# Kernel tuning notes

Hardware: AMD Instinct MI355X
Metric: run time of the kernel (lower is better)

The kernel has to match this reference:

```python
import jax, jax.numpy as jnp
import numpy as np

# Model config (matches init_kwargs)
V, SMAX, D, DH, H, M, L = 32000, 512, 512, 64, 8, 2048, 6
B, S, T = 4, 512, 512
PAD = 0

_SPEC = [
    ("tok_emb", (V, D), "n"), ("pos_emb", (SMAX, D), "n"),
    ("enc_ln1_w", (L, D), "1"), ("enc_ln1_b", (L, D), "0"),
    ("enc_wq", (L, H, D, DH), "n"), ("enc_wk", (L, H, D, DH), "n"), ("enc_wv", (L, H, D, DH), "n"),
    ("enc_wo", (L, H * DH, D), "n"), ("enc_bo", (L, D), "0"),
    ("enc_ln2_w", (L, D), "1"), ("enc_ln2_b", (L, D), "0"),
    ("enc_w1", (L, D, M), "n"), ("enc_b1", (L, M), "0"),
    ("enc_w2", (L, M, D), "n"), ("enc_b2", (L, D), "0"),
    ("enc_lnf_w", (D,), "1"), ("enc_lnf_b", (D,), "0"),
    ("dec_ln1_w", (L, D), "1"), ("dec_ln1_b", (L, D), "0"),
    ("dec_wq_s", (L, H, D, DH), "n"), ("dec_wk_s", (L, H, D, DH), "n"), ("dec_wv_s", (L, H, D, DH), "n"),
    ("dec_wo_s", (L, H * DH, D), "n"), ("dec_bo_s", (L, D), "0"),
    ("dec_ln2_w", (L, D), "1"), ("dec_ln2_b", (L, D), "0"),
    ("dec_wq_c", (L, H, D, DH), "n"), ("dec_wk_c", (L, H, D, DH), "n"), ("dec_wv_c", (L, H, D, DH), "n"),
    ("dec_wo_c", (L, H * DH, D), "n"), ("dec_bo_c", (L, D), "0"),
    ("dec_ln3_w", (L, D), "1"), ("dec_ln3_b", (L, D), "0"),
    ("dec_w1", (L, D, M), "n"), ("dec_b1", (L, M), "0"),
    ("dec_w2", (L, M, D), "n"), ("dec_b2", (L, D), "0"),
    ("dec_lnf_w", (D,), "1"), ("dec_lnf_b", (D,), "0"),
    ("head_w", (D, V), "n"), ("head_b", (V,), "0"),
]


def setup_inputs() -> dict:
    key = jax.random.key(0)
    k1, k2, key = jax.random.split(key, 3)
    inp = {
        "tokens_source": jax.random.randint(k1, (B, S), 0, V),
        "tokens_destination": jax.random.randint(k2, (B, T), 0, V),
    }
    for name, shape, kind in _SPEC:
        if kind == "n":
            key, k = jax.random.split(key)
            inp[name] = jax.random.normal(k, shape, jnp.float32) * 0.02
        elif kind == "1":
            inp[name] = jnp.ones(shape, jnp.float32)
        else:
            inp[name] = jnp.zeros(shape, jnp.float32)
    return inp


def _ln(x, w, b):
    mu = x.mean(-1, keepdims=True)
    var = ((x - mu) ** 2).mean(-1, keepdims=True)
    return (x - mu) * jax.lax.rsqrt(var + 1e-5) * w + b


def _mha(xq, xkv, wq, wk, wv, wo, bo, mask):
    # wq/wk/wv: [H, D, dh]; wo: [H*dh, D]; mask: bool [B or 1, Sq, Sk] (broadcast over heads)
    q = jnp.einsum("bsd,hde->bhse", xq, wq)
    k = jnp.einsum("btd,hde->bhte", xkv, wk)
    v = jnp.einsum("btd,hde->bhte", xkv, wv)
    scores = jnp.einsum("bhse,bhte->bhst", q, k) / (DH ** 0.5)
    scores = jnp.where(mask[:, None], scores, -jnp.inf)
    w = jax.nn.softmax(scores, axis=-1)
    o = jnp.einsum("bhst,bhte->bhse", w, v)
    b_, _, s_, _ = o.shape
    o = o.transpose(0, 2, 1, 3).reshape(b_, s_, H * DH)  # concat heads (head 0 first)
    return o @ wo + bo


def _forward(src, dst, p):
    s_, t_ = src.shape[1], dst.shape[1]
    key_mask = (src != PAD)[:, None, :]                      # [B,1,S]: mask over source keys
    causal = jnp.tril(jnp.ones((t_, t_), bool))[None]        # [1,T,T]
    x = p["tok_emb"][src] + p["pos_emb"][:s_]
    for i in range(L):
        h = _ln(x, p["enc_ln1_w"][i], p["enc_ln1_b"][i])
        x = x + _mha(h, h, p["enc_wq"][i], p["enc_wk"][i], p["enc_wv"][i], p["enc_wo"][i], p["enc_bo"][i], key_mask)
        h = _ln(x, p["enc_ln2_w"][i], p["enc_ln2_b"][i])
        x = x + jax.nn.gelu(h @ p["enc_w1"][i] + p["enc_b1"][i], approximate=False) @ p["enc_w2"][i] + p["enc_b2"][i]
    xe = _ln(x, p["enc_lnf_w"], p["enc_lnf_b"])
    y = p["tok_emb"][dst] + p["pos_emb"][:t_]
    for i in range(L):
        h = _ln(y, p["dec_ln1_w"][i], p["dec_ln1_b"][i])
        y = y + _mha(h, h, p["dec_wq_s"][i], p["dec_wk_s"][i], p["dec_wv_s"][i], p["dec_wo_s"][i], p["dec_bo_s"][i], causal)
        h = _ln(y, p["dec_ln2_w"][i], p["dec_ln2_b"][i])
        y = y + _mha(h, xe, p["dec_wq_c"][i], p["dec_wk_c"][i], p["dec_wv_c"][i], p["dec_wo_c"][i], p["dec_bo_c"][i], key_mask)
        h = _ln(y, p["dec_ln3_w"][i], p["dec_ln3_b"][i])
        y = y + jax.nn.gelu(h @ p["dec_w1"][i] + p["dec_b1"][i], approximate=False) @ p["dec_w2"][i] + p["dec_b2"][i]
    yd = _ln(y, p["dec_lnf_w"], p["dec_lnf_b"])
    return yd @ p["head_w"] + p["head_b"]  # logits [B, T, V]


def reference(tokens_source, tokens_destination, tok_emb, pos_emb, enc_ln1_w, enc_ln1_b, enc_wq, enc_wk, enc_wv, enc_wo, enc_bo, enc_ln2_w, enc_ln2_b, enc_w1, enc_b1, enc_w2, enc_b2, enc_lnf_w, enc_lnf_b, dec_ln1_w, dec_ln1_b, dec_wq_s, dec_wk_s, dec_wv_s, dec_wo_s, dec_bo_s, dec_ln2_w, dec_ln2_b, dec_wq_c, dec_wk_c, dec_wv_c, dec_wo_c, dec_bo_c, dec_ln3_w, dec_ln3_b, dec_w1, dec_b1, dec_w2, dec_b2, dec_lnf_w, dec_lnf_b, head_w, head_b):
    p = {k: v for k, v in locals().items() if k not in ("tokens_source", "tokens_destination")}
    return _forward(tokens_source, tokens_destination, p)
```

## Files before the change

### kernel.cpp

```cpp
#include <hip/hip_runtime.h>
#include <math.h>


typedef __bf16 bf16;
typedef bf16  bf16x8 __attribute__((ext_vector_type(8)));
typedef float f32x4  __attribute__((ext_vector_type(4)));

#define DEV __device__ __forceinline__

DEV f32x4 mfma16(bf16x8 a, bf16x8 b, f32x4 c) {
  return __builtin_amdgcn_mfma_f32_16x16x32_bf16(a, b, c, 0, 0, 0);
}

DEV void async_copy16(const bf16* g, bf16* l) {
  __builtin_amdgcn_global_load_lds(
      (__attribute__((address_space(1))) void*)(g),
      (__attribute__((address_space(3))) void*)(l), 16, 0, 0);
}

struct TJob { const float* in; bf16* out; long long oHi, oLo, oOfs; int R, C, zdiv, tile0; };
struct TJobs { TJob j[17]; };

__global__ __launch_bounds__(256) void tcast_all(TJobs JJ, int njobs)
{
  __shared__ float tile[32][33];
  const int t = blockIdx.x;
  int ji = 0;
#pragma unroll
  for (int k = 1; k < 17; ++k) if (k < njobs && JJ.j[k].tile0 <= t) ji = k;
  const TJob J = JJ.j[ji];
  const int rel  = t - J.tile0;
  const int ntx  = J.C >> 5, nty = J.R >> 5;
  const int perz = ntx * nty;
  const int z    = rel / perz;
  const int r2   = rel - z * perz;
  const int bx   = r2 % ntx, by = r2 / ntx;

  const long long zi = (long long)z * J.R * J.C;
  const long long zo = (long long)(z / J.zdiv) * J.oHi + (long long)(z % J.zdiv) * J.oLo + J.oOfs;
  const int c0 = bx * 32, r0 = by * 32;
  const int tx = threadIdx.x & 31, ty = (threadIdx.x >> 5);
#pragma unroll
  for (int i = 0; i < 32; i += 8)
    tile[ty + i][tx] = J.in[zi + (long long)(r0 + ty + i) * J.C + c0 + tx];
  __syncthreads();
#pragma unroll
  for (int i = 0; i < 32; i += 8)
    J.out[zo + (long long)(c0 + ty + i) * J.R + r0 + tx] = (bf16)tile[tx][ty + i];
}

__global__ __launch_bounds__(64) void embedln_kernel(
    const int* __restrict__ tok, const float* __restrict__ temb,
    const float* __restrict__ pemb, float* __restrict__ x,
    const float* __restrict__ w, const float* __restrict__ b,
    bf16* __restrict__ out)
{
  const int row  = blockIdx.x;
  const int sPos = row & 511;
  const int t    = tok[row];
  const int lane = threadIdx.x;
  const int c0   = lane * 8;
  f32x4 a0 = *(const f32x4*)&temb[(long long)t * 512 + c0];
  f32x4 a1 = *(const f32x4*)&temb[(long long)t * 512 + c0 + 4];
  f32x4 p0 = *(const f32x4*)&pemb[(long long)sPos * 512 + c0];
  f32x4 p1 = *(const f32x4*)&pemb[(long long)sPos * 512 + c0 + 4];
  a0 += p0; a1 += p1;
  *(f32x4*)&x[(long long)row * 512 + c0]     = a0;
  *(f32x4*)&x[(long long)row * 512 + c0 + 4] = a1;
  float s = 0.f, q = 0.f;
#pragma unroll
  for (int k = 0; k < 4; ++k) { s += a0[k] + a1[k]; q += a0[k]*a0[k] + a1[k]*a1[k]; }
#pragma unroll
  for (int m = 1; m < 64; m <<= 1) { s += __shfl_xor(s, m); q += __shfl_xor(q, m); }
  const float mean = s * (1.f / 512.f);
  const float var  = q * (1.f / 512.f) - mean * mean;
  const float rs   = rsqrtf(var + 1e-5f);
  f32x4 w0 = *(const f32x4*)&w[c0], w1 = *(const f32x4*)&w[c0 + 4];
  f32x4 b0 = *(const f32x4*)&b[c0], b1 = *(const f32x4*)&b[c0 + 4];
  bf16x8 o;
#pragma unroll
  for (int k = 0; k < 4; ++k) {
    o[k]     = (bf16)((a0[k] - mean) * rs * w0[k] + b0[k]);
    o[k + 4] = (bf16)((a1[k] - mean) * rs * w1[k] + b1[k]);
  }
  *(bf16x8*)&out[(long long)row * 512 + c0] = o;
}

__global__ __launch_bounds__(256) void addln_kernel(
    const bf16* __restrict__ g, const float* __restrict__ bias,
    float* __restrict__ x, const float* __restrict__ w,
    const float* __restrict__ bb, bf16* __restrict__ out)
{
  const int row  = blockIdx.x * 4 + (threadIdx.x >> 6);
  const int lane = threadIdx.x & 63;
  const int c0   = lane * 8;
  float* xr = x + (long long)row * 512;
  f32x4 a0 = *(const f32x4*)&xr[c0];
  f32x4 a1 = *(const f32x4*)&xr[c0 + 4];
  bf16x8 gv = *(const bf16x8*)&g[(long long)row * 512 + c0];
  f32x4 bi0 = *(const f32x4*)&bias[c0], bi1 = *(const f32x4*)&bias[c0 + 4];
  float v[8];
#pragma unroll
  for (int k = 0; k < 4; ++k) {
    v[k]     = a0[k] + (float)gv[k]     + bi0[k];
    v[k + 4] = a1[k] + (float)gv[k + 4] + bi1[k];
  }
  *(f32x4*)&xr[c0]     = f32x4{v[0], v[1], v[2], v[3]};
  *(f32x4*)&xr[c0 + 4] = f32x4{v[4], v[5], v[6], v[7]};
  float s = 0.f, q = 0.f;
#pragma unroll
  for (int k = 0; k < 8; ++k) { s += v[k]; q += v[k] * v[k]; }
#pragma unroll
  for (int m = 1; m < 64; m <<= 1) { s += __shfl_xor(s, m); q += __shfl_xor(q, m); }
  const float mean = s * (1.f / 512.f);
  const float var  = q * (1.f / 512.f) - mean * mean;
  const float rs   = rsqrtf(var + 1e-5f);
  f32x4 w0 = *(const f32x4*)&w[c0], w1 = *(const f32x4*)&w[c0 + 4];
  f32x4 b0 = *(const f32x4*)&bb[c0], b1 = *(const f32x4*)&bb[c0 + 4];
  bf16x8 o;
#pragma unroll
  for (int k = 0; k < 4; ++k) {
    o[k]     = (bf16)((v[k] - mean) * rs * w0[k] + b0[k]);
    o[k + 4] = (bf16)((v[k + 4] - mean) * rs * w1[k] + b1[k]);
  }
  *(bf16x8*)&out[(long long)row * 512 + c0] = o;
}

template <int MODE>
__global__ __launch_bounds__(64) void attn_kernel(
    const bf16* __restrict__ Q, const bf16* __restrict__ K,
    const bf16* __restrict__ Vt, bf16* __restrict__ O,
    const int* __restrict__ srctok)
{
  __shared__ bf16 Pw[16 * 68];
  const int bh = blockIdx.y;
  const int b  = bh >> 3;
  const int q0 = blockIdx.x * 16;
  const int ln = threadIdx.x;
  const int lr = ln & 15, g = ln >> 4;
  const bf16* Qg = Q + ((long long)bh * 512 + q0) * 64;
  const bf16* Kg = K + (long long)bh * 512 * 64;
  const bf16* Vg = Vt + (long long)bh * 64 * 512;
  const int* tkb = srctok + b * 512;

  const bf16x8 aq0 = *(const bf16x8*)&Qg[lr * 64 + g * 8];
  const bf16x8 aq1 = *(const bf16x8*)&Qg[lr * 64 + 32 + g * 8];

  float m[4] = {-1e30f, -1e30f, -1e30f, -1e30f};
  float l[4] = {0.f, 0.f, 0.f, 0.f};
  f32x4 o[4] = {};

  const int ktEnd = (MODE == 1) ? (q0 + 16) : 512;
  for (int kt = 0; kt < ktEnd; kt += 64) {
    bf16x8 bk[4][2], bv[4][2];
#pragma unroll
    for (int j = 0; j < 4; ++j) {
      bk[j][0] = *(const bf16x8*)&Kg[(long long)(kt + j * 16 + lr) * 64 + g * 8];
      bk[j][1] = *(const bf16x8*)&Kg[(long long)(kt + j * 16 + lr) * 64 + 32 + g * 8];
    }
#pragma unroll
    for (int n = 0; n < 4; ++n) {
      bv[n][0] = *(const bf16x8*)&Vg[(long long)(n * 16 + lr) * 512 + kt + g * 8];
      bv[n][1] = *(const bf16x8*)&Vg[(long long)(n * 16 + lr) * 512 + kt + 32 + g * 8];
    }
    f32x4 sf[4] = {};
#pragma unroll
    for (int j = 0; j < 4; ++j) {
      sf[j] = mfma16(aq0, bk[j][0], sf[j]);
      sf[j] = mfma16(aq1, bk[j][1], sf[j]);
    }
    float rm[4] = {-1e30f, -1e30f, -1e30f, -1e30f};
#pragma unroll
    for (int j = 0; j < 4; ++j) {
      if (MODE == 0) {
        const bool ok = (tkb[kt + j * 16 + lr] != 0);
#pragma unroll
        for (int r = 0; r < 4; ++r) if (!ok) sf[j][r] = -1e30f;
      } else {
        const int key = kt + j * 16 + lr;
#pragma unroll
        for (int r = 0; r < 4; ++r)
          if (key > q0 + g * 4 + r) sf[j][r] = -1e30f;
      }
#pragma unroll
      for (int r = 0; r < 4; ++r) rm[r] = fmaxf(rm[r], sf[j][r]);
    }
#pragma unroll
    for (int mk = 1; mk < 16; mk <<= 1)
#pragma unroll
      for (int r = 0; r < 4; ++r) rm[r] = fmaxf(rm[r], __shfl_xor(rm[r], mk));
    float al[4], ps[4] = {0.f, 0.f, 0.f, 0.f};
#pragma unroll
    for (int r = 0; r < 4; ++r) {
      const float mx = fmaxf(m[r], rm[r]);
      al[r] = __expf(m[r] - mx);
      m[r] = mx;
    }
#pragma unroll
    for (int j = 0; j < 4; ++j) {
#pragma unroll
      for (int r = 0; r < 4; ++r) {
        const float p = (sf[j][r] <= -1e29f) ? 0.f : __expf(sf[j][r] - m[r]);
        ps[r] += p;
        Pw[(g * 4 + r) * 68 + j * 16 + lr] = (bf16)p;
      }
    }
#pragma unroll
    for (int mk = 1; mk < 16; mk <<= 1)
#pragma unroll
      for (int r = 0; r < 4; ++r) ps[r] += __shfl_xor(ps[r], mk);
#pragma unroll
    for (int r = 0; r < 4; ++r) l[r] = l[r] * al[r] + ps[r];
#pragma unroll
    for (int n = 0; n < 4; ++n)
#pragma unroll
      for (int r = 0; r < 4; ++r) o[n][r] *= al[r];
#pragma unroll
    for (int ks = 0; ks < 2; ++ks) {
      const bf16x8 ap = *(const bf16x8*)&Pw[lr * 68 + ks * 32 + g * 8];
#pragma unroll
      for (int n = 0; n < 4; ++n)
        o[n] = mfma16(ap, bv[n][ks], o[n]);
    }
  }

#pragma unroll
  for (int r = 0; r < 4; ++r) {
    const float inv = 1.f / l[r];
    const long long gr = (long long)b * 512 + q0 + g * 4 + r;
#pragma unroll
    for (int n = 0; n < 4; ++n)
      O[gr * 512 + (bh & 7) * 64 + n * 16 + lr] = (bf16)(o[n][r] * inv);
  }
}

template <int BM, int BN, int EPI, bool SWZ = false>
__global__ __launch_bounds__(256) void gemm_kernel(
    const bf16* __restrict__ A, const bf16* __restrict__ Bw,
    void* __restrict__ Cc, const float* __restrict__ bias,
    const int K, const int lda, const int ldb, const int ldc,
    const long long sAz, const long long sBz,
    const long long sClo, const long long sChi, const int HB,
    const float scale)
{
  constexpr int BK = 64;
  __shared__ bf16 As[2][BM * BK];
  __shared__ bf16 Bs[2][BN * BK];
  constexpr int AISS = (BM * BK * 2) / 4096;
  constexpr int BISS = (BN * BK * 2) / 4096;

  const int z = blockIdx.z;
  const bf16* Az = A + (long long)z * sAz;
  const bf16* Bz = Bw + (long long)z * sBz;
  const long long cofs = (long long)(z % HB) * sClo + (long long)(z / HB) * sChi;

  const int tid  = threadIdx.x;
  const int wave = tid >> 6;
  const int lane = tid & 63;
  const int lr   = lane & 15;
  const int kg   = lane >> 4;

  int bx = blockIdx.x, by = blockIdx.y;
  if constexpr (SWZ) {
    const int nx = gridDim.x;
    const int nwg = nx * gridDim.y;
    const int id = by * nx + bx;
    const int chunk = nwg >> 3;
    const int swz = (id & 7) * chunk + (id >> 3);
    bx = swz % nx; by = swz / nx;
  }
  const int m0 = bx * BM;
  const int n0 = by * BN;

  constexpr int FM = BM / 32;
  constexpr int FN = BN / 32;
  const int wm = (wave >> 1) * (BM / 2);
  const int wn = (wave & 1) * (BN / 2);

  f32x4 acc[FM][FN] = {};

  auto stage = [&](int buf, int kt) {
#pragma unroll
    for (int i = 0; i < AISS; ++i) {
      const int o = i * 4096 + tid * 16;
      const int r = o >> 7;
      const int c = (o & 127) >> 1;
      async_copy16(Az + (long long)(m0 + r) * lda + kt + c, (bf16*)((char*)&As[buf][0] + o));
    }
#pragma unroll
    for (int i = 0; i < BISS; ++i) {
      const int o = i * 4096 + tid * 16;
      const int r = o >> 7;
      const int c = (o & 127) >> 1;
      async_copy16(Bz + (long long)(n0 + r) * ldb + kt + c, (bf16*)((char*)&Bs[buf][0] + o));
    }
  };

  const int NT = K / BK;
  stage(0, 0);
  asm volatile("s_waitcnt vmcnt(0)" ::: "memory");
  __builtin_amdgcn_s_barrier();
  __builtin_amdgcn_sched_barrier(0);

  int cur = 0;
  for (int t = 0; t < NT; ++t) {
    if (t + 1 < NT) stage(cur ^ 1, (t + 1) * BK);
#pragma unroll
    for (int ks = 0; ks < 2; ++ks) {
      bf16x8 af[FM], bq[FN];
#pragma unroll
      for (int i = 0; i < FM; ++i)
        af[i] = *(const bf16x8*)&As[cur][(wm + i * 16 + lr) * BK + ks * 32 + kg * 8];
#pragma unroll
      for (int j = 0; j < FN; ++j)
        bq[j] = *(const bf16x8*)&Bs[cur][(wn + j * 16 + lr) * BK + ks * 32 + kg * 8];
#pragma unroll
      for (int i = 0; i < FM; ++i)
#pragma unroll
        for (int j = 0; j < FN; ++j)
          acc[i][j] = mfma16(af[i], bq[j], acc[i][j]);
    }
    if (t + 1 < NT) {
      asm volatile("s_waitcnt vmcnt(0) lgkmcnt(0)" ::: "memory");
      __builtin_amdgcn_s_barrier();
      __builtin_amdgcn_sched_barrier(0);
      cur ^= 1;
    }
  }

#pragma unroll
  for (int i = 0; i < FM; ++i) {
#pragma unroll
    for (int j = 0; j < FN; ++j) {
      const int gc = n0 + wn + j * 16 + lr;
#pragma unroll
      for (int r = 0; r < 4; ++r) {
        const int gr = m0 + wm + i * 16 + kg * 4 + r;
        const float v = acc[i][j][r];
        if constexpr (EPI == 0) {
          ((bf16*)Cc + cofs)[(long long)gr * ldc + gc] = (bf16)v;
        } else if constexpr (EPI == 3) {
          float t = v + bias[gc];
          t = 0.5f * t * (1.f + erff(t * 0.70710678118654752f));
          ((bf16*)Cc)[(long long)gr * ldc + gc] = (bf16)t;
        } else if constexpr (EPI == 4) {
          __builtin_nontemporal_store(v + bias[gc], &((float*)Cc)[(long long)gr * ldc + gc]);
        } else if constexpr (EPI == 7) {
          const int sel = gc >> 9;
          const int hh = (gc >> 6) & 7, ee = gc & 63;
          const int bb = gr >> 9, ss = gr & 511;
          bf16* base = (bf16*)Cc + (long long)sel * (2048 * 512);
          const float vv = (sel == 0) ? v * 0.125f : v;
          if (sel < 2) base[(((long long)(bb * 8 + hh) << 9) + ss) * 64 + ee] = (bf16)vv;
          else         base[(((long long)(bb * 8 + hh) << 6) + ee) * 512 + ss] = (bf16)vv;
        } else if constexpr (EPI == 8) {
          const int sel = gc >> 9;
          const int hh = (gc >> 6) & 7, ee = gc & 63;
          const int bb = gr >> 9, ss = gr & 511;
          bf16* base = (bf16*)Cc + (long long)z * sChi + (long long)sel * (2048 * 512);
          if (sel == 0) base[(((long long)(bb * 8 + hh) << 9) + ss) * 64 + ee] = (bf16)v;
          else          base[(((long long)(bb * 8 + hh) << 6) + ee) * 512 + ss] = (bf16)v;
        }
      }
    }
  }
}

extern "C" void kernel_launch(void* const* d_in, const int* in_sizes, int n_in,
                              void* d_out, int out_size, void* d_ws, size_t ws_size,
                              hipStream_t stream)
{
  const int*   tok_src   = (const int*)d_in[0];
  const int*   tok_dst   = (const int*)d_in[1];
  const float* tok_emb   = (const float*)d_in[2];
  const float* pos_emb   = (const float*)d_in[3];
  const float* enc_ln1_w = (const float*)d_in[4];
  const float* enc_ln1_b = (const float*)d_in[5];
  const float* enc_wq    = (const float*)d_in[6];
  const float* enc_wk    = (const float*)d_in[7];
  const float* enc_wv    = (const float*)d_in[8];
  const float* enc_wo    = (const float*)d_in[9];
  const float* enc_bo    = (const float*)d_in[10];
  const float* enc_ln2_w = (const float*)d_in[11];
  const float* enc_ln2_b = (const float*)d_in[12];
  const float* enc_w1    = (const float*)d_in[13];
  const float* enc_b1    = (const float*)d_in[14];
  const float* enc_w2    = (const float*)d_in[15];
  const float* enc_b2    = (const float*)d_in[16];
  const float* enc_lnf_w = (const float*)d_in[17];
  const float* enc_lnf_b = (const float*)d_in[18];
  const float* dec_ln1_w = (const float*)d_in[19];
  const float* dec_ln1_b = (const float*)d_in[20];
  const float* dec_wq_s  = (const float*)d_in[21];
  const float* dec_wk_s  = (const float*)d_in[22];
  const float* dec_wv_s  = (const float*)d_in[23];
  const float* dec_wo_s  = (const float*)d_in[24];
  const float* dec_bo_s  = (const float*)d_in[25];
  const float* dec_ln2_w = (const float*)d_in[26];
  const float* dec_ln2_b = (const float*)d_in[27];
  const float* dec_wq_c  = (const float*)d_in[28];
  const float* dec_wk_c  = (const float*)d_in[29];
  const float* dec_wv_c  = (const float*)d_in[30];
  const float* dec_wo_c  = (const float*)d_in[31];
  const float* dec_bo_c  = (const float*)d_in[32];
  const float* dec_ln3_w = (const float*)d_in[33];
  const float* dec_ln3_b = (const float*)d_in[34];
  const float* dec_w1    = (const float*)d_in[35];
  const float* dec_b1    = (const float*)d_in[36];
  const float* dec_w2    = (const float*)d_in[37];
  const float* dec_b2    = (const float*)d_in[38];
  const float* dec_lnf_w = (const float*)d_in[39];
  const float* dec_lnf_b = (const float*)d_in[40];
  const float* head_w    = (const float*)d_in[41];
  const float* head_b    = (const float*)d_in[42];
  float* outp = (float*)d_out;

  char* wp = (char*)d_ws;
  auto alloc = [&](size_t nbytes) -> char* {
    char* p = wp; wp += (nbytes + 255) & ~(size_t)255; return p;
  };
  const long long LQKV = 1536LL * 512;
  const long long LKV  = 1024LL * 512;
  const long long LSQ  = 512LL * 512;
  const long long LFF  = 2048LL * 512;
  const long long KVST = 2LL * 2048 * 512;

  bf16* tQKV_e = (bf16*)alloc((size_t)6 * LQKV * 2);
  bf16* tQKV_s = (bf16*)alloc((size_t)6 * LQKV * 2);
  bf16* tQ_c   = (bf16*)alloc((size_t)6 * LSQ * 2);
  bf16* tKV_c  = (bf16*)alloc((size_t)6 * LKV * 2);
  bf16* tWo_e  = (bf16*)alloc((size_t)6 * LSQ * 2);
  bf16* tWo_s  = (bf16*)alloc((size_t)6 * LSQ * 2);
  bf16* tWo_c  = (bf16*)alloc((size_t)6 * LSQ * 2);
  bf16* tW1_e  = (bf16*)alloc((size_t)6 * LFF * 2);
  bf16* tW2_e  = (bf16*)alloc((size_t)6 * LFF * 2);
  bf16* tW1_d  = (bf16*)alloc((size_t)6 * LFF * 2);
  bf16* tW2_d  = (bf16*)alloc((size_t)6 * LFF * 2);
  bf16* tHead  = (bf16*)alloc((size_t)32000 * 512 * 2);

  float* x   = (float*)alloc((size_t)2048 * 512 * 4);
  float* y   = (float*)alloc((size_t)2048 * 512 * 4);
  bf16*  h   = (bf16*)alloc((size_t)2048 * 512 * 2);
  bf16*  qkv = (bf16*)alloc((size_t)3 * 2048 * 512 * 2);
  bf16*  xe  = (bf16*)alloc((size_t)2048 * 512 * 2);
  bf16*  kvc = (bf16*)alloc((size_t)6 * KVST * 2);
  bf16*  ob  = (bf16*)alloc((size_t)2048 * 512 * 2);
  bf16*  t0  = (bf16*)alloc((size_t)2048 * 512 * 2);
  bf16*  h1  = (bf16*)alloc((size_t)2048 * 2048 * 2);
  bf16*  yd  = (bf16*)alloc((size_t)2048 * 512 * 2);

  bf16* ql = qkv;
  bf16* kl = qkv + 2048 * 512;
  bf16* vt = qkv + 2 * 2048 * 512;

  TJobs JJ; int nt = 0, nj = 0;
  auto addjob = [&](const float* in, bf16* out, int R, int C,
                    long long oHi, long long oLo, int zdiv, long long oOfs, int nz) {
    JJ.j[nj] = TJob{in, out, oHi, oLo, oOfs, R, C, zdiv, nt};
    nt += (C / 32) * (R / 32) * nz; ++nj;
  };
  addjob(enc_wq,   tQKV_e, 512, 64,   LQKV, 32768, 8, 0,      48);
  addjob(enc_wk,   tQKV_e, 512, 64,   LQKV, 32768, 8, 262144, 48);
  addjob(enc_wv,   tQKV_e, 512, 64,   LQKV, 32768, 8, 524288, 48);
  addjob(dec_wq_s, tQKV_s, 512, 64,   LQKV, 32768, 8, 0,      48);
  addjob(dec_wk_s, tQKV_s, 512, 64,   LQKV, 32768, 8, 262144, 48);
  addjob(dec_wv_s, tQKV_s, 512, 64,   LQKV, 32768, 8, 524288, 48);
  addjob(dec_wq_c, tQ_c,   512, 64,   LSQ,  32768, 8, 0,      48);
  addjob(dec_wk_c, tKV_c,  512, 64,   LKV,  32768, 8, 0,      48);
  addjob(dec_wv_c, tKV_c,  512, 64,   LKV,  32768, 8, 262144, 48);
  addjob(enc_wo,   tWo_e,  512, 512,  LSQ,  0, 1, 0, 6);
  addjob(dec_wo_s, tWo_s,  512, 512,  LSQ,  0, 1, 0, 6);
  addjob(dec_wo_c, tWo_c,  512, 512,  LSQ,  0, 1, 0, 6);
  addjob(enc_w1,   tW1_e,  512, 2048, LFF,  0, 1, 0, 6);
  addjob(enc_w2,   tW2_e,  2048, 512, LFF,  0, 1, 0, 6);
  addjob(dec_w1,   tW1_d,  512, 2048, LFF,  0, 1, 0, 6);
  addjob(dec_w2,   tW2_d,  2048, 512, LFF,  0, 1, 0, 6);
  addjob(head_w,   tHead,  512, 32000, 0,   0, 1, 0, 1);
  tcast_all<<<nt, 256, 0, stream>>>(JJ, nj);

  embedln_kernel<<<2048, 64, 0, stream>>>(tok_src, tok_emb, pos_emb, x, enc_ln1_w, enc_ln1_b, h);
  for (int l = 0; l < 6; ++l) {
    gemm_kernel<64, 128, 7><<<dim3(32, 12, 1), 256, 0, stream>>>(
        h, tQKV_e + (size_t)l * LQKV, qkv, nullptr, 512, 512, 512, 0, 0, 0, 0, 0, 1, 1.f);
    attn_kernel<0><<<dim3(32, 32), 64, 0, stream>>>(ql, kl, vt, ob, tok_src);
    gemm_kernel<64, 64, 0><<<dim3(32, 8, 1), 256, 0, stream>>>(
        ob, tWo_e + (size_t)l * LSQ, t0, nullptr, 512, 512, 512, 512, 0, 0, 0, 0, 1, 1.f);
    addln_kernel<<<512, 256, 0, stream>>>(t0, enc_bo + l * 512, x,
        enc_ln2_w + l * 512, enc_ln2_b + l * 512, h);
    gemm_kernel<64, 128, 3><<<dim3(32, 16, 1), 256, 0, stream>>>(
        h, tW1_e + (size_t)l * LFF, h1, enc_b1 + l * 2048, 512, 512, 512, 2048, 0, 0, 0, 0, 1, 1.f);
    gemm_kernel<64, 64, 0><<<dim3(32, 8, 1), 256, 0, stream>>>(
        h1, tW2_e + (size_t)l * LFF, t0, nullptr, 2048, 2048, 2048, 512, 0, 0, 0, 0, 1, 1.f);
    const float* nw = (l < 5) ? enc_ln1_w + (l + 1) * 512 : enc_lnf_w;
    const float* nb = (l < 5) ? enc_ln1_b + (l + 1) * 512 : enc_lnf_b;
    addln_kernel<<<512, 256, 0, stream>>>(t0, enc_b2 + l * 512, x, nw, nb, (l < 5) ? h : xe);
  }

  gemm_kernel<128, 128, 8><<<dim3(16, 8, 6), 256, 0, stream>>>(
      xe, tKV_c, kvc, nullptr, 512, 512, 512, 0, 0, LKV, 0, KVST, 1, 1.f);

  embedln_kernel<<<2048, 64, 0, stream>>>(tok_dst, tok_emb, pos_emb, y, dec_ln1_w, dec_ln1_b, h);
  for (int l = 0; l < 6; ++l) {
    gemm_kernel<64, 128, 7><<<dim3(32, 12, 1), 256, 0, stream>>>(
        h, tQKV_s + (size_t)l * LQKV, qkv, nullptr, 512, 512, 512, 0, 0, 0, 0, 0, 1, 1.f);
    attn_kernel<1><<<dim3(32, 32), 64, 0, stream>>>(ql, kl, vt, ob, nullptr);
    gemm_kernel<64, 64, 0><<<dim3(32, 8, 1), 256, 0, stream>>>(
        ob, tWo_s + (size_t)l * LSQ, t0, nullptr, 512, 512, 512, 512, 0, 0, 0, 0, 1, 1.f);
    addln_kernel<<<512, 256, 0, stream>>>(t0, dec_bo_s + l * 512, y,
        dec_ln2_w + l * 512, dec_ln2_b + l * 512, h);
    gemm_kernel<64, 64, 7><<<dim3(32, 8, 1), 256, 0, stream>>>(
        h, tQ_c + (size_t)l * LSQ, qkv, nullptr, 512, 512, 512, 0, 0, 0, 0, 0, 1, 1.f);
    attn_kernel<0><<<dim3(32, 32), 64, 0, stream>>>(
        ql, kvc + (size_t)l * KVST, kvc + (size_t)l * KVST + 2048 * 512, ob, tok_src);
    gemm_kernel<64, 64, 0><<<dim3(32, 8, 1), 256, 0, stream>>>(
        ob, tWo_c + (size_t)l * LSQ, t0, nullptr, 512, 512, 512, 512, 0, 0, 0, 0, 1, 1.f);
    addln_kernel<<<512, 256, 0, stream>>>(t0, dec_bo_c + l * 512, y,
        dec_ln3_w + l * 512, dec_ln3_b + l * 512, h);
    gemm_kernel<64, 128, 3><<<dim3(32, 16, 1), 256, 0, stream>>>(
        h, tW1_d + (size_t)l * LFF, h1, dec_b1 + l * 2048, 512, 512, 512, 2048, 0, 0, 0, 0, 1, 1.f);
    gemm_kernel<64, 64, 0><<<dim3(32, 8, 1), 256, 0, stream>>>(
        h1, tW2_d + (size_t)l * LFF, t0, nullptr, 2048, 2048, 2048, 512, 0, 0, 0, 0, 1, 1.f);
    const float* nw = (l < 5) ? dec_ln1_w + (l + 1) * 512 : dec_lnf_w;
    const float* nb = (l < 5) ? dec_ln1_b + (l + 1) * 512 : dec_lnf_b;
    addln_kernel<<<512, 256, 0, stream>>>(t0, dec_b2 + l * 512, y, nw, nb, (l < 5) ? h : yd);
  }
  gemm_kernel<128, 128, 4, true><<<dim3(16, 250, 1), 256, 0, stream>>>(
      yd, tHead, outp, head_b, 512, 512, 512, 32000, 0, 0, 0, 0, 1, 1.f);
}
```

Before: 2.144 ms.

## Split-K output GEMMs into fp32 partials, shrink tiles, widen attention blocks

The Wo and W2 projection GEMMs now use split-K (2 or 4 slices), writing fp32 partial sums that the add+LayerNorm kernel adds together. This gives more blocks on the small-N GEMMs and drops the bf16 rounding of their outputs. The other GEMMs move to 32-row tiles for more blocks, attention processes 128 keys per iteration instead of 64, and the encoder and decoder embedding+LN are merged into one launch, with the decoder result staged in yd and copied to h later. The cost is extra partial-buffer traffic and higher register pressure in attention.

```diff
diff --git a/kernel.cpp b/kernel.cpp
--- a/kernel.cpp
+++ b/kernel.cpp
@@ -49,13 +49,22 @@
     J.out[zo + (long long)(c0 + ty + i) * J.R + r0 + tx] = (bf16)tile[tx][ty + i];
 }
 
-__global__ __launch_bounds__(64) void embedln_kernel(
-    const int* __restrict__ tok, const float* __restrict__ temb,
-    const float* __restrict__ pemb, float* __restrict__ x,
-    const float* __restrict__ w, const float* __restrict__ b,
-    bf16* __restrict__ out)
+__global__ __launch_bounds__(64) void embedln2_kernel(
+    const int* __restrict__ tokA, const int* __restrict__ tokB,
+    const float* __restrict__ temb, const float* __restrict__ pemb,
+    float* __restrict__ xA, float* __restrict__ xB,
+    const float* __restrict__ wA, const float* __restrict__ bA,
+    const float* __restrict__ wB, const float* __restrict__ bB,
+    bf16* __restrict__ outA, bf16* __restrict__ outB)
 {
-  const int row  = blockIdx.x;
+  const bool sB = blockIdx.x >= 2048;
+  const int row = sB ? blockIdx.x - 2048 : blockIdx.x;
+  const int* tok = sB ? tokB : tokA;
+  float* x = sB ? xB : xA;
+  const float* w = sB ? wB : wA;
+  const float* b = sB ? bB : bA;
+  bf16* out = sB ? outB : outA;
+
   const int sPos = row & 511;
   const int t    = tok[row];
   const int lane = threadIdx.x;
@@ -86,8 +95,9 @@
   *(bf16x8*)&out[(long long)row * 512 + c0] = o;
 }
 
+template <int P>
 __global__ __launch_bounds__(256) void addln_kernel(
-    const bf16* __restrict__ g, const float* __restrict__ bias,
+    const float* __restrict__ part, const float* __restrict__ bias,
     float* __restrict__ x, const float* __restrict__ w,
     const float* __restrict__ bb, bf16* __restrict__ out)
 {
@@ -97,19 +107,19 @@
   float* xr = x + (long long)row * 512;
   f32x4 a0 = *(const f32x4*)&xr[c0];
   f32x4 a1 = *(const f32x4*)&xr[c0 + 4];
-  bf16x8 gv = *(const bf16x8*)&g[(long long)row * 512 + c0];
+#pragma unroll
+  for (int p = 0; p < P; ++p) {
+    const float* pr = part + (long long)p * (2048 * 512) + (long long)row * 512;
+    a0 += *(const f32x4*)&pr[c0];
+    a1 += *(const f32x4*)&pr[c0 + 4];
+  }
   f32x4 bi0 = *(const f32x4*)&bias[c0], bi1 = *(const f32x4*)&bias[c0 + 4];
-  float v[8];
-#pragma unroll
-  for (int k = 0; k < 4; ++k) {
-    v[k]     = a0[k] + (float)gv[k]     + bi0[k];
-    v[k + 4] = a1[k] + (float)gv[k + 4] + bi1[k];
-  }
-  *(f32x4*)&xr[c0]     = f32x4{v[0], v[1], v[2], v[3]};
-  *(f32x4*)&xr[c0 + 4] = f32x4{v[4], v[5], v[6], v[7]};
+  a0 += bi0; a1 += bi1;
+  *(f32x4*)&xr[c0]     = a0;
+  *(f32x4*)&xr[c0 + 4] = a1;
   float s = 0.f, q = 0.f;
 #pragma unroll
-  for (int k = 0; k < 8; ++k) { s += v[k]; q += v[k] * v[k]; }
+  for (int k = 0; k < 4; ++k) { s += a0[k] + a1[k]; q += a0[k]*a0[k] + a1[k]*a1[k]; }
 #pragma unroll
   for (int m = 1; m < 64; m <<= 1) { s += __shfl_xor(s, m); q += __shfl_xor(q, m); }
   const float mean = s * (1.f / 512.f);
@@ -120,8 +130,8 @@
   bf16x8 o;
 #pragma unroll
   for (int k = 0; k < 4; ++k) {
-    o[k]     = (bf16)((v[k] - mean) * rs * w0[k] + b0[k]);
-    o[k + 4] = (bf16)((v[k + 4] - mean) * rs * w1[k] + b1[k]);
+    o[k]     = (bf16)((a0[k] - mean) * rs * w0[k] + b0[k]);
+    o[k + 4] = (bf16)((a1[k] - mean) * rs * w1[k] + b1[k]);
   }
   *(bf16x8*)&out[(long long)row * 512 + c0] = o;
 }
@@ -132,7 +142,7 @@
     const bf16* __restrict__ Vt, bf16* __restrict__ O,
     const int* __restrict__ srctok)
 {
-  __shared__ bf16 Pw[16 * 68];
+  __shared__ bf16 Pw[16 * 136];
   const int bh = blockIdx.y;
   const int b  = bh >> 3;
   const int q0 = blockIdx.x * 16;
@@ -151,27 +161,28 @@
   f32x4 o[4] = {};
 
   const int ktEnd = (MODE == 1) ? (q0 + 16) : 512;
-  for (int kt = 0; kt < ktEnd; kt += 64) {
-    bf16x8 bk[4][2], bv[4][2];
-#pragma unroll
-    for (int j = 0; j < 4; ++j) {
+  for (int kt = 0; kt < ktEnd; kt += 128) {
+    bf16x8 bk[8][2], bv[4][4];
+#pragma unroll
+    for (int j = 0; j < 8; ++j) {
       bk[j][0] = *(const bf16x8*)&Kg[(long long)(kt + j * 16 + lr) * 64 + g * 8];
       bk[j][1] = *(const bf16x8*)&Kg[(long long)(kt + j * 16 + lr) * 64 + 32 + g * 8];
     }
 #pragma unroll
-    for (int n = 0; n < 4; ++n) {
-      bv[n][0] = *(const bf16x8*)&Vg[(long long)(n * 16 + lr) * 512 + kt + g * 8];
-      bv[n][1] = *(const bf16x8*)&Vg[(long long)(n * 16 + lr) * 512 + kt + 32 + g * 8];
-    }
-    f32x4 sf[4] = {};
-#pragma unroll
-    for (int j = 0; j < 4; ++j) {
+    for (int n = 0; n < 4; ++n)
+#pragma unroll
+      for (int ks = 0; ks < 4; ++ks)
+        bv[n][ks] = *(const bf16x8*)&Vg[(long long)(n * 16 + lr) * 512 + kt + ks * 32 + g * 8];
+
+    f32x4 sf[8] = {};
+#pragma unroll
+    for (int j = 0; j < 8; ++j) {
       sf[j] = mfma16(aq0, bk[j][0], sf[j]);
       sf[j] = mfma16(aq1, bk[j][1], sf[j]);
     }
     float rm[4] = {-1e30f, -1e30f, -1e30f, -1e30f};
 #pragma unroll
-    for (int j = 0; j < 4; ++j) {
+    for (int j = 0; j < 8; ++j) {
       if (MODE == 0) {
         const bool ok = (tkb[kt + j * 16 + lr] != 0);
 #pragma unroll
@@ -197,12 +208,12 @@
       m[r] = mx;
     }
 #pragma unroll
-    for (int j = 0; j < 4; ++j) {
+    for (int j = 0; j < 8; ++j) {
 #pragma unroll
       for (int r = 0; r < 4; ++r) {
         const float p = (sf[j][r] <= -1e29f) ? 0.f : __expf(sf[j][r] - m[r]);
         ps[r] += p;
-        Pw[(g * 4 + r) * 68 + j * 16 + lr] = (bf16)p;
+        Pw[(g * 4 + r) * 136 + j * 16 + lr] = (bf16)p;
       }
     }
 #pragma unroll
@@ -216,8 +227,8 @@
 #pragma unroll
       for (int r = 0; r < 4; ++r) o[n][r] *= al[r];
 #pragma unroll
-    for (int ks = 0; ks < 2; ++ks) {
-      const bf16x8 ap = *(const bf16x8*)&Pw[lr * 68 + ks * 32 + g * 8];
+    for (int ks = 0; ks < 4; ++ks) {
+      const bf16x8 ap = *(const bf16x8*)&Pw[lr * 136 + ks * 32 + g * 8];
 #pragma unroll
       for (int n = 0; n < 4; ++n)
         o[n] = mfma16(ap, bv[n][ks], o[n]);
@@ -337,9 +348,7 @@
       for (int r = 0; r < 4; ++r) {
         const int gr = m0 + wm + i * 16 + kg * 4 + r;
         const float v = acc[i][j][r];
-        if constexpr (EPI == 0) {
-          ((bf16*)Cc + cofs)[(long long)gr * ldc + gc] = (bf16)v;
-        } else if constexpr (EPI == 3) {
+        if constexpr (EPI == 3) {
           float t = v + bias[gc];
           t = 0.5f * t * (1.f + erff(t * 0.70710678118654752f));
           ((bf16*)Cc)[(long long)gr * ldc + gc] = (bf16)t;
@@ -360,6 +369,8 @@
           bf16* base = (bf16*)Cc + (long long)z * sChi + (long long)sel * (2048 * 512);
           if (sel == 0) base[(((long long)(bb * 8 + hh) << 9) + ss) * 64 + ee] = (bf16)v;
           else          base[(((long long)(bb * 8 + hh) << 6) + ee) * 512 + ss] = (bf16)v;
+        } else if constexpr (EPI == 9) {
+          ((float*)Cc)[cofs + (long long)gr * ldc + gc] = v;
         }
       }
     }
@@ -424,6 +435,7 @@
   const long long LSQ  = 512LL * 512;
   const long long LFF  = 2048LL * 512;
   const long long KVST = 2LL * 2048 * 512;
+  const long long PSTR = 2048LL * 512;
 
   bf16* tQKV_e = (bf16*)alloc((size_t)6 * LQKV * 2);
   bf16* tQKV_s = (bf16*)alloc((size_t)6 * LQKV * 2);
@@ -438,16 +450,16 @@
   bf16* tW2_d  = (bf16*)alloc((size_t)6 * LFF * 2);
   bf16* tHead  = (bf16*)alloc((size_t)32000 * 512 * 2);
 
-  float* x   = (float*)alloc((size_t)2048 * 512 * 4);
-  float* y   = (float*)alloc((size_t)2048 * 512 * 4);
-  bf16*  h   = (bf16*)alloc((size_t)2048 * 512 * 2);
-  bf16*  qkv = (bf16*)alloc((size_t)3 * 2048 * 512 * 2);
-  bf16*  xe  = (bf16*)alloc((size_t)2048 * 512 * 2);
-  bf16*  kvc = (bf16*)alloc((size_t)6 * KVST * 2);
-  bf16*  ob  = (bf16*)alloc((size_t)2048 * 512 * 2);
-  bf16*  t0  = (bf16*)alloc((size_t)2048 * 512 * 2);
-  bf16*  h1  = (bf16*)alloc((size_t)2048 * 2048 * 2);
-  bf16*  yd  = (bf16*)alloc((size_t)2048 * 512 * 2);
+  float* x    = (float*)alloc((size_t)2048 * 512 * 4);
+  float* y    = (float*)alloc((size_t)2048 * 512 * 4);
+  bf16*  h    = (bf16*)alloc((size_t)2048 * 512 * 2);
+  bf16*  qkv  = (bf16*)alloc((size_t)3 * 2048 * 512 * 2);
+  bf16*  xe   = (bf16*)alloc((size_t)2048 * 512 * 2);
+  bf16*  kvc  = (bf16*)alloc((size_t)6 * KVST * 2);
+  bf16*  ob   = (bf16*)alloc((size_t)2048 * 512 * 2);
+  float* part = (float*)alloc((size_t)4 * PSTR * 4);
+  bf16*  h1   = (bf16*)alloc((size_t)2048 * 2048 * 2);
+  bf16*  yd   = (bf16*)alloc((size_t)2048 * 512 * 2);
 
   bf16* ql = qkv;
   bf16* kl = qkv + 2048 * 512;
@@ -478,51 +490,55 @@
   addjob(head_w,   tHead,  512, 32000, 0,   0, 1, 0, 1);
   tcast_all<<<nt, 256, 0, stream>>>(JJ, nj);
 
-  embedln_kernel<<<2048, 64, 0, stream>>>(tok_src, tok_emb, pos_emb, x, enc_ln1_w, enc_ln1_b, h);
+  embedln2_kernel<<<4096, 64, 0, stream>>>(tok_src, tok_dst, tok_emb, pos_emb,
+      x, y, enc_ln1_w, enc_ln1_b, dec_ln1_w, dec_ln1_b, h, yd);
+
   for (int l = 0; l < 6; ++l) {
-    gemm_kernel<64, 128, 7><<<dim3(32, 12, 1), 256, 0, stream>>>(
+    gemm_kernel<32, 128, 7><<<dim3(64, 12, 1), 256, 0, stream>>>(
         h, tQKV_e + (size_t)l * LQKV, qkv, nullptr, 512, 512, 512, 0, 0, 0, 0, 0, 1, 1.f);
     attn_kernel<0><<<dim3(32, 32), 64, 0, stream>>>(ql, kl, vt, ob, tok_src);
-    gemm_kernel<64, 64, 0><<<dim3(32, 8, 1), 256, 0, stream>>>(
-        ob, tWo_e + (size_t)l * LSQ, t0, nullptr, 512, 512, 512, 512, 0, 0, 0, 0, 1, 1.f);
-    addln_kernel<<<512, 256, 0, stream>>>(t0, enc_bo + l * 512, x,
+    gemm_kernel<32, 64, 9><<<dim3(64, 8, 2), 256, 0, stream>>>(
+        ob, tWo_e + (size_t)l * LSQ, part, nullptr, 256, 512, 512, 512, 256, 256, 0, PSTR, 1, 1.f);
+    addln_kernel<2><<<512, 256, 0, stream>>>(part, enc_bo + l * 512, x,
         enc_ln2_w + l * 512, enc_ln2_b + l * 512, h);
-    gemm_kernel<64, 128, 3><<<dim3(32, 16, 1), 256, 0, stream>>>(
+    gemm_kernel<32, 128, 3><<<dim3(64, 16, 1), 256, 0, stream>>>(
         h, tW1_e + (size_t)l * LFF, h1, enc_b1 + l * 2048, 512, 512, 512, 2048, 0, 0, 0, 0, 1, 1.f);
-    gemm_kernel<64, 64, 0><<<dim3(32, 8, 1), 256, 0, stream>>>(
-        h1, tW2_e + (size_t)l * LFF, t0, nullptr, 2048, 2048, 2048, 512, 0, 0, 0, 0, 1, 1.f);
+    gemm_kernel<32, 64, 9><<<dim3(64, 8, 4), 256, 0, stream>>>(
+        h1, tW2_e + (size_t)l * LFF, part, nullptr, 512, 2048, 2048, 512, 512, 512, 0, PSTR, 1, 1.f);
     const float* nw = (l < 5) ? enc_ln1_w + (l + 1) * 512 : enc_lnf_w;
     const float* nb = (l < 5) ? enc_ln1_b + (l + 1) * 512 : enc_lnf_b;
-    addln_kernel<<<512, 256, 0, stream>>>(t0, enc_b2 + l * 512, x, nw, nb, (l < 5) ? h : xe);
+    addln_kernel<4><<<512, 256, 0, stream>>>(part, enc_b2 + l * 512, x, nw, nb, (l < 5) ? h : xe);
   }
 
   gemm_kernel<128, 128, 8><<<dim3(16, 8, 6), 256, 0, stream>>>(
       xe, tKV_c, kvc, nullptr, 512, 512, 512, 0, 0, LKV, 0, KVST, 1, 1.f);
 
-  embedln_kernel<<<2048, 64, 0, stream>>>(tok_dst, tok_emb, pos_emb, y, dec_ln1_w, dec_ln1_b, h);
+  {
+    hipMemcpyAsync(h, yd, (size_t)2048 * 512 * 2, hipMemcpyDeviceToDevice, stream);
+  }
   for (int l = 0; l < 6; ++l) {
-    gemm_kernel<64, 128, 7><<<dim3(32, 12, 1), 256, 0, stream>>>(
+    gemm_kernel<32, 128, 7><<<dim3(64, 12, 1), 256, 0, stream>>>(
         h, tQKV_s + (size_t)l * LQKV, qkv, nullptr, 512, 512, 512, 0, 0, 0, 0, 0, 1, 1.f);
     attn_kernel<1><<<dim3(32, 32), 64, 0, stream>>>(ql, kl, vt, ob, nullptr);
-    gemm_kernel<64, 64, 0><<<dim3(32, 8, 1), 256, 0, stream>>>(
-        ob, tWo_s + (size_t)l * LSQ, t0, nullptr, 512, 512, 512, 512, 0, 0, 0, 0, 1, 1.f);
-    addln_kernel<<<512, 256, 0, stream>>>(t0, dec_bo_s + l * 512, y,
+    gemm_kernel<32, 64, 9><<<dim3(64, 8, 2), 256, 0, stream>>>(
+        ob, tWo_s + (size_t)l * LSQ, part, nullptr, 256, 512, 512, 512, 256, 256, 0, PSTR, 1, 1.f);
+    addln_kernel<2><<<512, 256, 0, stream>>>(part, dec_bo_s + l * 512, y,
         dec_ln2_w + l * 512, dec_ln2_b + l * 512, h);
-    gemm_kernel<64, 64, 7><<<dim3(32, 8, 1), 256, 0, stream>>>(
+    gemm_kernel<32, 64, 7><<<dim3(64, 8, 1), 256, 0, stream>>>(
         h, tQ_c + (size_t)l * LSQ, qkv, nullptr, 512, 512, 512, 0, 0, 0, 0, 0, 1, 1.f);
     attn_kernel<0><<<dim3(32, 32), 64, 0, stream>>>(
         ql, kvc + (size_t)l * KVST, kvc + (size_t)l * KVST + 2048 * 512, ob, tok_src);
-    gemm_kernel<64, 64, 0><<<dim3(32, 8, 1), 256, 0, stream>>>(
-        ob, tWo_c + (size_t)l * LSQ, t0, nullptr, 512, 512, 512, 512, 0, 0, 0, 0, 1, 1.f);
-    addln_kernel<<<512, 256, 0, stream>>>(t0, dec_bo_c + l * 512, y,
+    gemm_kernel<32, 64, 9><<<dim3(64, 8, 2), 256, 0, stream>>>(
+        ob, tWo_c + (size_t)l * LSQ, part, nullptr, 256, 512, 512, 512, 256, 256, 0, PSTR, 1, 1.f);
+    addln_kernel<2><<<512, 256, 0, stream>>>(part, dec_bo_c + l * 512, y,
         dec_ln3_w + l * 512, dec_ln3_b + l * 512, h);
-    gemm_kernel<64, 128, 3><<<dim3(32, 16, 1), 256, 0, stream>>>(
+    gemm_kernel<32, 128, 3><<<dim3(64, 16, 1), 256, 0, stream>>>(
         h, tW1_d + (size_t)l * LFF, h1, dec_b1 + l * 2048, 512, 512, 512, 2048, 0, 0, 0, 0, 1, 1.f);
-    gemm_kernel<64, 64, 0><<<dim3(32, 8, 1), 256, 0, stream>>>(
-        h1, tW2_d + (size_t)l * LFF, t0, nullptr, 2048, 2048, 2048, 512, 0, 0, 0, 0, 1, 1.f);
+    gemm_kernel<32, 64, 9><<<dim3(64, 8, 4), 256, 0, stream>>>(
+        h1, tW2_d + (size_t)l * LFF, part, nullptr, 512, 2048, 2048, 512, 512, 512, 0, PSTR, 1, 1.f);
     const float* nw = (l < 5) ? dec_ln1_w + (l + 1) * 512 : dec_lnf_w;
     const float* nb = (l < 5) ? dec_ln1_b + (l + 1) * 512 : dec_lnf_b;
-    addln_kernel<<<512, 256, 0, stream>>>(t0, dec_b2 + l * 512, y, nw, nb, (l < 5) ? h : yd);
+    addln_kernel<4><<<512, 256, 0, stream>>>(part, dec_b2 + l * 512, y, nw, nb, (l < 5) ? h : yd);
   }
   gemm_kernel<128, 128, 4, true><<<dim3(16, 250, 1), 256, 0, stream>>>(
       yd, tHead, outp, head_b, 512, 512, 512, 32000, 0, 0, 0, 0, 1, 1.f);
```

After: 2.033 ms. 1.05x faster.
